# Optimization experiments

Hardware: AMD Instinct MI355X
Metric: run time of the kernel (lower is better)

Reference implementation:

```python
import jax, jax.numpy as jnp
import numpy as np

B, N, C = 16, 65536, 21          # batch, anchors, classes (class 0 = background)
TH_CONF = 0.05                   # confidence threshold
TH_IOU = 0.5                     # NMS IoU threshold
TOP_K = 200                      # candidates kept per (batch, class) before NMS
V0, V1 = 0.1, 0.2                # SSD box-coder variances


def setup_inputs() -> dict:
    key = jax.random.key(0)
    k1, k2, k3, k4 = jax.random.split(key, 4)
    conf = jax.random.normal(k1, (B, N, C), dtype=jnp.float32)
    loc = jax.random.normal(k2, (B, N, 4), dtype=jnp.float32)
    # anchors in center form (cx, cy, w, h), normalized coords
    cxcy = jax.random.uniform(k3, (N, 2), dtype=jnp.float32)
    wh = 0.02 + 0.2 * jax.random.uniform(k4, (N, 2), dtype=jnp.float32)
    anchors = jnp.concatenate([cxcy, wh], axis=-1)
    return {"conf": conf, "loc": loc, "anchors": anchors}


def _decode(anchors, loc):
    # SSD decode: anchors [N,4] center form, loc [B,N,4] offsets -> [B,N,4] xyxy
    a_xy, a_wh = anchors[:, :2], anchors[:, 2:]
    xy = a_xy + loc[..., :2] * V0 * a_wh
    wh = a_wh * jnp.exp(loc[..., 2:] * V1)
    return jnp.concatenate([xy - 0.5 * wh, xy + 0.5 * wh], axis=-1)


def _iou(boxes):
    # boxes [K,4] xyxy -> pairwise IoU [K,K]
    area = jnp.maximum(boxes[:, 2] - boxes[:, 0], 0.0) * jnp.maximum(boxes[:, 3] - boxes[:, 1], 0.0)
    lt = jnp.maximum(boxes[:, None, :2], boxes[None, :, :2])
    rb = jnp.minimum(boxes[:, None, 2:], boxes[None, :, 2:])
    wh = jnp.maximum(rb - lt, 0.0)
    inter = wh[..., 0] * wh[..., 1]
    union = area[:, None] + area[None, :] - inter
    return inter / jnp.maximum(union, 1e-9)


def _nms_keep(iou, valid):
    # greedy NMS over score-sorted candidates; valid = (score >= TH_CONF)
    K = iou.shape[0]
    idx = jnp.arange(K)

    def body(keep, xs):
        row, v, i = xs
        suppressed = jnp.any((row > TH_IOU) & keep & (idx < i))
        k = v & (~suppressed)
        return keep.at[i].set(k), 0

    keep, _ = jax.lax.scan(body, jnp.zeros((K,), dtype=bool), (iou, valid, idx))
    return keep


def reference(conf, loc, anchors):
    score = jax.nn.softmax(conf, axis=2)            # [B,N,C]
    boxes = _decode(anchors, loc)                   # [B,N,4]
    # skip background class 0 (cls_base = 1 for softmax classifier)
    cls_scores = jnp.swapaxes(score[..., 1:], 1, 2)  # [B,C-1,N]
    top_s, top_i = jax.lax.top_k(cls_scores, TOP_K)  # [B,C-1,K], sorted desc
    top_boxes = jax.vmap(lambda bx, ix: bx[ix])(boxes, top_i)  # [B,C-1,K,4]
    valid = top_s >= TH_CONF
    keep = jax.vmap(jax.vmap(lambda b, v: _nms_keep(_iou(b), v)))(top_boxes, valid)  # [B,C-1,K]
    out_boxes = jnp.where(keep[..., None], top_boxes, 0.0)
    out_scores = jnp.where(keep, top_s, 0.0)
    return jnp.concatenate([out_boxes, out_scores[..., None]], axis=-1)  # [B,C-1,K,5]
```

## Files before the change

kernel.cpp:

```cpp
#include <hip/hip_runtime.h>
#include <stdint.h>

#define NB     16
#define NANCH  65536
#define NC     21
#define NCLS   20
#define NCOL   (NB * NCLS)
#define TOPK   200
#define NBINS  2048
#define CAP    256
#define CAPCOL 4096

constexpr float TH      = 0.05f;
constexpr float TPRE    = 0.15f;
constexpr float SCALE15 = (float)NBINS / 0.85f;
constexpr float SCALE05 = (float)NBINS / 0.95f;

__device__ __forceinline__ int bin15(float s) {
  int b = (int)((s - 0.15f) * SCALE15);
  return b < 0 ? 0 : (b > NBINS - 1 ? NBINS - 1 : b);
}
__device__ __forceinline__ int bin05(float s) {
  int b = (int)((s - 0.05f) * SCALE05);
  return b < 0 ? 0 : (b > NBINS - 1 ? NBINS - 1 : b);
}

__device__ __forceinline__ unsigned long long shflx64(unsigned long long v, int m) {
  unsigned int lo = (unsigned int)v, hi = (unsigned int)(v >> 32);
  lo = __shfl_xor(lo, m);
  hi = __shfl_xor(hi, m);
  return ((unsigned long long)hi << 32) | lo;
}

__device__ __forceinline__ void softmax_tail(const float* x, float* e, float& S) {
  float m = x[0];
#pragma unroll
  for (int c = 1; c < NC; ++c) m = fmaxf(m, x[c]);
#pragma unroll
  for (int c = 0; c < NC; ++c) e[c] = expf(x[c] - m);
  float r0 = e[0] + e[8],  r1 = e[1] + e[9],  r2 = e[2] + e[10], r3 = e[3] + e[11];
  float r4 = e[4] + e[12], r5 = e[5] + e[13], r6 = e[6] + e[14], r7 = e[7] + e[15];
  S = ((r0 + r1) + (r2 + r3)) + ((r4 + r5) + (r6 + r7));
  S += e[16]; S += e[17]; S += e[18]; S += e[19]; S += e[20];
}

__global__ __launch_bounds__(256) void softmax_collect_kernel(
    const float* __restrict__ conf,
    unsigned int* __restrict__ cnt, unsigned long long* __restrict__ cand) {
  const int tid = threadIdx.x;
  __shared__ float ld[256 * NC];
  const float4* src = (const float4*)conf + (long long)blockIdx.x * 1344;
  float4* dst4 = (float4*)ld;
#pragma unroll
  for (int i = 0; i < 5; ++i) dst4[tid + i * 256] = src[tid + i * 256];
  if (tid < 64) dst4[tid + 1280] = src[tid + 1280];
  __syncthreads();

  const int a = blockIdx.x * 256 + tid;
  const int b = a >> 16;
  const int n = a & (NANCH - 1);
  float x[NC];
#pragma unroll
  for (int c = 0; c < NC; ++c) x[c] = ld[tid * NC + c];
  float e[NC], S;
  softmax_tail(x, e, S);
  float sc[NCLS];
  unsigned int takemask = 0;
#pragma unroll
  for (int c = 0; c < NCLS; ++c) {
    sc[c] = e[c + 1] / S;
    if (sc[c] >= TPRE) takemask |= (1u << c);
  }

  __shared__ unsigned int wcnt[4][NCLS];
  __shared__ unsigned int wbase[4][NCLS];
  const int wave = tid >> 6, lane = tid & 63;
#pragma unroll
  for (int c = 0; c < NCLS; ++c) {
    unsigned long long m = __ballot((takemask >> c) & 1);
    if (lane == 0) wcnt[wave][c] = (unsigned int)__popcll(m);
  }
  __syncthreads();
  if (tid < NCLS) {
    const int c = tid;
    unsigned int t0 = wcnt[0][c], t1 = wcnt[1][c], t2 = wcnt[2][c], t3 = wcnt[3][c];
    unsigned int tot = t0 + t1 + t2 + t3;
    unsigned int base = tot ? atomicAdd(&cnt[b * NCLS + c], tot) : 0u;
    wbase[0][c] = base;
    wbase[1][c] = base + t0;
    wbase[2][c] = base + t0 + t1;
    wbase[3][c] = base + t0 + t1 + t2;
  }
  __syncthreads();
#pragma unroll
  for (int c = 0; c < NCLS; ++c) {
    bool take = (takemask >> c) & 1;
    unsigned long long m = __ballot(take);
    if (take) {
      unsigned int off = wbase[wave][c] +
                         (unsigned int)__popcll(m & ((1ULL << lane) - 1));
      if (off < CAPCOL) {
        unsigned int key = __float_as_uint(sc[c]) | 0x80000000u;
        cand[(long long)(b * NCLS + c) * CAPCOL + off] =
            ((unsigned long long)(key ^ 0xFFFFFFFFu) << 32) |
            (unsigned long long)(unsigned int)n;
      }
    }
  }
}

__device__ __forceinline__ int find_sel(unsigned int* hist, unsigned int* part,
                                        int* s_sel, int tid) {
  unsigned int p = 0;
#pragma unroll
  for (int i = 0; i < 8; ++i) p += hist[tid * 8 + i];
  part[tid] = p;
  if (tid == 0) *s_sel = -1;
  __syncthreads();
  if (tid < 64) {
    unsigned int p4 = part[tid * 4] + part[tid * 4 + 1] +
                      part[tid * 4 + 2] + part[tid * 4 + 3];
    unsigned int sfx = p4;
#pragma unroll
    for (int off = 1; off < 64; off <<= 1) {
      unsigned int o = __shfl_down(sfx, off);
      if (tid + off < 64) sfx += o;
    }
    unsigned int above = sfx - p4;
    if (above < TOPK && sfx >= TOPK) {
      unsigned int cum = above; int sel = tid * 32; bool found = false;
      for (int q = 3; q >= 0 && !found; --q) {
        unsigned int pc = part[tid * 4 + q];
        if (cum + pc >= TOPK) {
          for (int i = 7; i >= 0; --i) {
            unsigned int c = hist[(tid * 4 + q) * 8 + i];
            if (cum + c >= TOPK) { sel = (tid * 4 + q) * 8 + i; found = true; break; }
            cum += c;
          }
        } else cum += pc;
      }
      *s_sel = sel;
    }
  }
  __syncthreads();
  return *s_sel;
}

__global__ __launch_bounds__(256) void topk_nms_kernel(
    const unsigned long long* __restrict__ candg,
    const unsigned int* __restrict__ cnt,
    const float* __restrict__ conf, const float* __restrict__ loc,
    const float* __restrict__ anchors, float* __restrict__ out) {
  const int bc = blockIdx.x;
  const int b  = bc / NCLS;
  const int cls = bc % NCLS;
  const int tid = threadIdx.x;

  __shared__ unsigned long long cg_lds[CAPCOL];
  __shared__ unsigned int hist[NBINS];
  __shared__ unsigned int part[256];
  __shared__ int s_sel, s_n;
  __shared__ unsigned long long cand[CAP];
  __shared__ float bx[TOPK][5];
  __shared__ float barea[TOPK];
  __shared__ unsigned long long adj[TOPK][4];
  __shared__ unsigned char keepf[TOPK];

  int nc = (int)cnt[bc];
  const bool fast = (nc >= TOPK && nc <= CAPCOL);
  for (int i = tid; i < NBINS; i += 256) hist[i] = 0;
  if (tid == 0) s_n = 0;
  __syncthreads();

  if (fast) {
    const unsigned long long* cg = candg + (long long)bc * CAPCOL;
    for (int i = tid; i < nc; i += 256) {
      unsigned long long k64 = cg[i];
      cg_lds[i] = k64;
      unsigned int key = (unsigned int)(k64 >> 32) ^ 0xFFFFFFFFu;
      float s = __uint_as_float(key ^ 0x80000000u);
      atomicAdd(&hist[bin15(s)], 1u);
    }
    __syncthreads();
    int sel = find_sel(hist, part, &s_sel, tid);
    for (int i = tid; i < nc; i += 256) {
      unsigned long long k64 = cg_lds[i];
      unsigned int key = (unsigned int)(k64 >> 32) ^ 0xFFFFFFFFu;
      float s = __uint_as_float(key ^ 0x80000000u);
      if (bin15(s) >= sel) {
        int pos = atomicAdd(&s_n, 1);
        if (pos < CAP) cand[pos] = k64;
      }
    }
  } else {
    for (int n = tid; n < NANCH; n += 256) {
      const float* row = conf + ((long long)b * NANCH + n) * NC;
      float x[NC], e[NC], S;
#pragma unroll
      for (int c = 0; c < NC; ++c) x[c] = row[c];
      softmax_tail(x, e, S);
      float s = e[cls + 1] / S;
      if (s >= TH) atomicAdd(&hist[bin05(s)], 1u);
    }
    __syncthreads();
    int sel = find_sel(hist, part, &s_sel, tid);
    for (int n = tid; n < NANCH; n += 256) {
      const float* row = conf + ((long long)b * NANCH + n) * NC;
      float x[NC], e[NC], S;
#pragma unroll
      for (int c = 0; c < NC; ++c) x[c] = row[c];
      softmax_tail(x, e, S);
      float s = e[cls + 1] / S;
      if (s >= TH && (sel < 0 || bin05(s) >= sel)) {
        int pos = atomicAdd(&s_n, 1);
        if (pos < CAP) {
          unsigned int key = __float_as_uint(s) | 0x80000000u;
          cand[pos] = ((unsigned long long)(key ^ 0xFFFFFFFFu) << 32) |
                      (unsigned long long)(unsigned int)n;
        }
      }
    }
  }
  __syncthreads();
  int ncand = s_n; if (ncand > CAP) ncand = CAP;

  unsigned long long v = (tid < ncand) ? cand[tid] : ~0ULL;
  for (int k = 2; k <= CAP; k <<= 1) {
    const bool up = ((tid & k) == 0);
    for (int j = k >> 1; j >= 64; j >>= 1) {
      cand[tid] = v;
      __syncthreads();
      unsigned long long o = cand[tid ^ j];
      bool keepMin = (((tid & j) == 0) == up);
      v = ((v < o) == keepMin) ? v : o;
      __syncthreads();
    }
    for (int j = (k >> 1) < 32 ? (k >> 1) : 32; j >= 1; j >>= 1) {
      unsigned long long o = shflx64(v, j);
      bool keepMin = (((tid & j) == 0) == up);
      v = ((v < o) == keepMin) ? v : o;
    }
  }
  const int nsel = (ncand < TOPK) ? ncand : TOPK;

  if (tid < TOPK) {
    if (tid < nsel) {
      unsigned int key = (unsigned int)(v >> 32) ^ 0xFFFFFFFFu;
      float s = __uint_as_float(key ^ 0x80000000u);
      int idx = (int)(unsigned int)(v & 0xFFFFFFFFu);
      float4 anc = ((const float4*)anchors)[idx];
      float4 l   = ((const float4*)loc)[(long long)b * NANCH + idx];
      float cx = anc.x + (l.x * 0.1f) * anc.z;
      float cy = anc.y + (l.y * 0.1f) * anc.w;
      float w  = anc.z * expf(l.z * 0.2f);
      float h  = anc.w * expf(l.w * 0.2f);
      float x1 = cx - 0.5f * w, y1 = cy - 0.5f * h;
      float x2 = cx + 0.5f * w, y2 = cy + 0.5f * h;
      bx[tid][0] = x1; bx[tid][1] = y1; bx[tid][2] = x2; bx[tid][3] = y2;
      bx[tid][4] = s;
      barea[tid] = fmaxf(x2 - x1, 0.0f) * fmaxf(y2 - y1, 0.0f);
    } else {
      bx[tid][0] = bx[tid][1] = bx[tid][2] = bx[tid][3] = bx[tid][4] = 0.0f;
      barea[tid] = 0.0f;
    }
  }
  __syncthreads();

  if (tid < TOPK) {
    float ax1 = bx[tid][0], ay1 = bx[tid][1], ax2 = bx[tid][2], ay2 = bx[tid][3];
    float aar = barea[tid];
    for (int w = 0; w < 4; ++w) {
      unsigned long long mword = 0;
      int lim = (w < 3) ? 64 : (TOPK - 192);
      for (int jj = 0; jj < lim; ++jj) {
        int j = (w << 6) + jj;
        float ltx = fmaxf(ax1, bx[j][0]);
        float lty = fmaxf(ay1, bx[j][1]);
        float rbx = fminf(ax2, bx[j][2]);
        float rby = fminf(ay2, bx[j][3]);
        float iw = fmaxf(rbx - ltx, 0.0f);
        float ih = fmaxf(rby - lty, 0.0f);
        float inter = iw * ih;
        float uni = aar + barea[j] - inter;
        float iou = inter / fmaxf(uni, 1e-9f);
        if (iou > 0.5f) mword |= (1ULL << jj);
      }
      adj[tid][w] = mword;
    }
  }
  __syncthreads();

  if (tid == 0) {
    unsigned long long s0 = 0, s1 = 0, s2 = 0, s3 = 0;
    for (int i = 0; i < 64; ++i) {
      unsigned long long m0 = adj[i][0], m1 = adj[i][1],
                         m2 = adj[i][2], m3 = adj[i][3];
      bool kept = (i < nsel) && !((s0 >> i) & 1ULL);
      keepf[i] = kept ? 1 : 0;
      if (kept) { s0 |= m0; s1 |= m1; s2 |= m2; s3 |= m3; }
    }
    for (int i = 64; i < 128; ++i) {
      unsigned long long m0 = adj[i][0], m1 = adj[i][1],
                         m2 = adj[i][2], m3 = adj[i][3];
      bool kept = (i < nsel) && !((s1 >> (i - 64)) & 1ULL);
      keepf[i] = kept ? 1 : 0;
      if (kept) { s0 |= m0; s1 |= m1; s2 |= m2; s3 |= m3; }
    }
    for (int i = 128; i < 192; ++i) {
      unsigned long long m0 = adj[i][0], m1 = adj[i][1],
                         m2 = adj[i][2], m3 = adj[i][3];
      bool kept = (i < nsel) && !((s2 >> (i - 128)) & 1ULL);
      keepf[i] = kept ? 1 : 0;
      if (kept) { s0 |= m0; s1 |= m1; s2 |= m2; s3 |= m3; }
    }
    for (int i = 192; i < TOPK; ++i) {
      unsigned long long m0 = adj[i][0], m1 = adj[i][1],
                         m2 = adj[i][2], m3 = adj[i][3];
      bool kept = (i < nsel) && !((s3 >> (i - 192)) & 1ULL);
      keepf[i] = kept ? 1 : 0;
      if (kept) { s0 |= m0; s1 |= m1; s2 |= m2; s3 |= m3; }
    }
  }
  __syncthreads();

  if (tid < TOPK) {
    float* o = out + ((long long)bc * TOPK + tid) * 5;
    bool k = keepf[tid] != 0;
    o[0] = k ? bx[tid][0] : 0.0f;
    o[1] = k ? bx[tid][1] : 0.0f;
    o[2] = k ? bx[tid][2] : 0.0f;
    o[3] = k ? bx[tid][3] : 0.0f;
    o[4] = k ? bx[tid][4] : 0.0f;
  }
}

extern "C" void kernel_launch(void* const* d_in, const int* in_sizes, int n_in,
                              void* d_out, int out_size, void* d_ws, size_t ws_size,
                              hipStream_t stream) {
  const float* conf    = (const float*)d_in[0];
  const float* loc     = (const float*)d_in[1];
  const float* anchors = (const float*)d_in[2];
  float* out = (float*)d_out;

  char* ws = (char*)d_ws;
  unsigned long long* cand = (unsigned long long*)ws;
  unsigned int*       cnt  = (unsigned int*)(ws + 10485760);

  hipMemsetAsync(ws + 10485760, 0, 1280, stream);
  softmax_collect_kernel<<<(NB * NANCH) / 256, 256, 0, stream>>>(conf, cnt, cand);
  topk_nms_kernel<<<NCOL, 256, 0, stream>>>(cand, cnt, conf, loc, anchors, out);
}
```

Before: 108.6 us.

## Trim softmax divides, pad counters, wave-aggregate compaction, upper-triangle IoU

In the collect kernel, the threshold test now compares exp values against TPRE*S, so the per-class divide only happens for classes that pass. The per-column global counters are padded to 16-word stride to reduce atomic contention on shared cache lines. In the top-k kernel the histogram shrinks to 1024 bins, the LDS staging of candidates is dropped in favour of re-reading global memory, and compaction uses one wave-aggregated atomic per wave. The IoU adjacency build only computes the upper triangle (j > i) and skips most divides with a tolerance-guarded comparison, at the cost of extra branches and a possible coarser threshold bin.

```diff
diff --git a/kernel.cpp b/kernel.cpp
--- a/kernel.cpp
+++ b/kernel.cpp
@@ -7,9 +7,10 @@
 #define NCLS   20
 #define NCOL   (NB * NCLS)
 #define TOPK   200
-#define NBINS  2048
+#define NBINS  1024
 #define CAP    256
 #define CAPCOL 4096
+#define CNTSTRIDE 16
 
 constexpr float TH      = 0.05f;
 constexpr float TPRE    = 0.15f;
@@ -64,13 +65,11 @@
   for (int c = 0; c < NC; ++c) x[c] = ld[tid * NC + c];
   float e[NC], S;
   softmax_tail(x, e, S);
-  float sc[NCLS];
+  const float t = TPRE * S;
   unsigned int takemask = 0;
 #pragma unroll
-  for (int c = 0; c < NCLS; ++c) {
-    sc[c] = e[c + 1] / S;
-    if (sc[c] >= TPRE) takemask |= (1u << c);
-  }
+  for (int c = 0; c < NCLS; ++c)
+    if (e[c + 1] >= t) takemask |= (1u << c);
 
   __shared__ unsigned int wcnt[4][NCLS];
   __shared__ unsigned int wbase[4][NCLS];
@@ -85,7 +84,7 @@
     const int c = tid;
     unsigned int t0 = wcnt[0][c], t1 = wcnt[1][c], t2 = wcnt[2][c], t3 = wcnt[3][c];
     unsigned int tot = t0 + t1 + t2 + t3;
-    unsigned int base = tot ? atomicAdd(&cnt[b * NCLS + c], tot) : 0u;
+    unsigned int base = tot ? atomicAdd(&cnt[(b * NCLS + c) * CNTSTRIDE], tot) : 0u;
     wbase[0][c] = base;
     wbase[1][c] = base + t0;
     wbase[2][c] = base + t0 + t1;
@@ -97,10 +96,11 @@
     bool take = (takemask >> c) & 1;
     unsigned long long m = __ballot(take);
     if (take) {
+      float s = e[c + 1] / S;
       unsigned int off = wbase[wave][c] +
                          (unsigned int)__popcll(m & ((1ULL << lane) - 1));
       if (off < CAPCOL) {
-        unsigned int key = __float_as_uint(sc[c]) | 0x80000000u;
+        unsigned int key = __float_as_uint(s) | 0x80000000u;
         cand[(long long)(b * NCLS + c) * CAPCOL + off] =
             ((unsigned long long)(key ^ 0xFFFFFFFFu) << 32) |
             (unsigned long long)(unsigned int)n;
@@ -111,15 +111,12 @@
 
 __device__ __forceinline__ int find_sel(unsigned int* hist, unsigned int* part,
                                         int* s_sel, int tid) {
-  unsigned int p = 0;
-#pragma unroll
-  for (int i = 0; i < 8; ++i) p += hist[tid * 8 + i];
+  unsigned int p = hist[tid*4] + hist[tid*4+1] + hist[tid*4+2] + hist[tid*4+3];
   part[tid] = p;
   if (tid == 0) *s_sel = -1;
   __syncthreads();
   if (tid < 64) {
-    unsigned int p4 = part[tid * 4] + part[tid * 4 + 1] +
-                      part[tid * 4 + 2] + part[tid * 4 + 3];
+    unsigned int p4 = part[tid*4] + part[tid*4+1] + part[tid*4+2] + part[tid*4+3];
     unsigned int sfx = p4;
 #pragma unroll
     for (int off = 1; off < 64; off <<= 1) {
@@ -128,13 +125,13 @@
     }
     unsigned int above = sfx - p4;
     if (above < TOPK && sfx >= TOPK) {
-      unsigned int cum = above; int sel = tid * 32; bool found = false;
+      unsigned int cum = above; int sel = tid * 16; bool found = false;
       for (int q = 3; q >= 0 && !found; --q) {
-        unsigned int pc = part[tid * 4 + q];
+        unsigned int pc = part[tid*4 + q];
         if (cum + pc >= TOPK) {
-          for (int i = 7; i >= 0; --i) {
-            unsigned int c = hist[(tid * 4 + q) * 8 + i];
-            if (cum + c >= TOPK) { sel = (tid * 4 + q) * 8 + i; found = true; break; }
+          for (int i = 3; i >= 0; --i) {
+            unsigned int c = hist[(tid*4+q)*4 + i];
+            if (cum + c >= TOPK) { sel = (tid*4+q)*4 + i; found = true; break; }
             cum += c;
           }
         } else cum += pc;
@@ -155,8 +152,8 @@
   const int b  = bc / NCLS;
   const int cls = bc % NCLS;
   const int tid = threadIdx.x;
-
-  __shared__ unsigned long long cg_lds[CAPCOL];
+  const int lane = tid & 63;
+
   __shared__ unsigned int hist[NBINS];
   __shared__ unsigned int part[256];
   __shared__ int s_sel, s_n;
@@ -166,29 +163,38 @@
   __shared__ unsigned long long adj[TOPK][4];
   __shared__ unsigned char keepf[TOPK];
 
-  int nc = (int)cnt[bc];
+  int nc = (int)cnt[bc * CNTSTRIDE];
   const bool fast = (nc >= TOPK && nc <= CAPCOL);
   for (int i = tid; i < NBINS; i += 256) hist[i] = 0;
   if (tid == 0) s_n = 0;
   __syncthreads();
 
+  const unsigned long long* cg = candg + (long long)bc * CAPCOL;
   if (fast) {
-    const unsigned long long* cg = candg + (long long)bc * CAPCOL;
     for (int i = tid; i < nc; i += 256) {
-      unsigned long long k64 = cg[i];
-      cg_lds[i] = k64;
-      unsigned int key = (unsigned int)(k64 >> 32) ^ 0xFFFFFFFFu;
+      unsigned int key = (unsigned int)(cg[i] >> 32) ^ 0xFFFFFFFFu;
       float s = __uint_as_float(key ^ 0x80000000u);
       atomicAdd(&hist[bin15(s)], 1u);
     }
     __syncthreads();
     int sel = find_sel(hist, part, &s_sel, tid);
-    for (int i = tid; i < nc; i += 256) {
-      unsigned long long k64 = cg_lds[i];
-      unsigned int key = (unsigned int)(k64 >> 32) ^ 0xFFFFFFFFu;
-      float s = __uint_as_float(key ^ 0x80000000u);
-      if (bin15(s) >= sel) {
-        int pos = atomicAdd(&s_n, 1);
+    const int ncr = (nc + 255) & ~255;
+    for (int i = tid; i < ncr; i += 256) {
+      bool have = i < nc;
+      unsigned long long k64 = have ? cg[i] : 0ULL;
+      bool takeit = false;
+      if (have) {
+        unsigned int key = (unsigned int)(k64 >> 32) ^ 0xFFFFFFFFu;
+        float s = __uint_as_float(key ^ 0x80000000u);
+        takeit = bin15(s) >= sel;
+      }
+      unsigned long long m = __ballot(takeit);
+      int cw = (int)__popcll(m);
+      int base = 0;
+      if (lane == 0 && cw) base = atomicAdd(&s_n, cw);
+      base = __shfl(base, 0);
+      if (takeit) {
+        int pos = base + (int)__popcll(m & ((1ULL << lane) - 1));
         if (pos < CAP) cand[pos] = k64;
       }
     }
@@ -269,11 +275,12 @@
   if (tid < TOPK) {
     float ax1 = bx[tid][0], ay1 = bx[tid][1], ax2 = bx[tid][2], ay2 = bx[tid][3];
     float aar = barea[tid];
+#pragma unroll
     for (int w = 0; w < 4; ++w) {
       unsigned long long mword = 0;
-      int lim = (w < 3) ? 64 : (TOPK - 192);
-      for (int jj = 0; jj < lim; ++jj) {
-        int j = (w << 6) + jj;
+      int jlo = w * 64; if (jlo < tid + 1) jlo = tid + 1;
+      int jhi = w * 64 + 64; if (jhi > TOPK) jhi = TOPK;
+      for (int j = jlo; j < jhi; ++j) {
         float ltx = fmaxf(ax1, bx[j][0]);
         float lty = fmaxf(ay1, bx[j][1]);
         float rbx = fminf(ax2, bx[j][2]);
@@ -282,8 +289,13 @@
         float ih = fmaxf(rby - lty, 0.0f);
         float inter = iw * ih;
         float uni = aar + barea[j] - inter;
-        float iou = inter / fmaxf(uni, 1e-9f);
-        if (iou > 0.5f) mword |= (1ULL << jj);
+        float um = fmaxf(uni, 1e-9f);
+        float half = 0.5f * um;
+        bool hit;
+        if (inter > half * 1.000001f)      hit = true;
+        else if (inter < half * 0.999999f) hit = false;
+        else                               hit = (inter / um > 0.5f);
+        if (hit) mword |= (1ULL << (j - w * 64));
       }
       adj[tid][w] = mword;
     }
@@ -346,7 +358,7 @@
   unsigned long long* cand = (unsigned long long*)ws;
   unsigned int*       cnt  = (unsigned int*)(ws + 10485760);
 
-  hipMemsetAsync(ws + 10485760, 0, 1280, stream);
+  hipMemsetAsync(ws + 10485760, 0, 320 * CNTSTRIDE * 4, stream);
   softmax_collect_kernel<<<(NB * NANCH) / 256, 256, 0, stream>>>(conf, cnt, cand);
   topk_nms_kernel<<<NCOL, 256, 0, stream>>>(cand, cnt, conf, loc, anchors, out);
 }
```

Result: slower. 117.8 us (+8.5%).
